# Kernel optimization log

Measured on AMD Instinct MI355X. Metric: run time of the kernel, lower is better.

## Reference

```python
import jax, jax.numpy as jnp
import numpy as np

N = 50000      # num nodes
E = 800000     # num edges (before self-loops)
DIN = 256
DOUT = 256
K = 3


def setup_inputs() -> dict:
    key = jax.random.key(0)
    k1, k2, k3 = jax.random.split(key, 3)
    x = jax.random.normal(k1, (N, DIN), dtype=jnp.float32)
    edge_index = jax.random.randint(k2, (2, E), 0, N, dtype=jnp.int32)
    # xavier_uniform for weight [K+1, DIN, DOUT]
    limit = float(np.sqrt(6.0 / (DIN + DOUT)))
    weight = jax.random.uniform(k3, (K + 1, DIN, DOUT), dtype=jnp.float32,
                                minval=-limit, maxval=limit)
    bias = jnp.zeros((DOUT,), dtype=jnp.float32)
    return {"x": x, "edge_index": edge_index, "weight": weight, "bias": bias}


def reference(x, edge_index, weight, bias):
    num_nodes = x.shape[0]
    # add self loops
    loops = jnp.arange(num_nodes, dtype=edge_index.dtype)
    row = jnp.concatenate([edge_index[0], loops])
    col = jnp.concatenate([edge_index[1], loops])
    # degree of row (including self loops)
    deg = jax.ops.segment_sum(jnp.ones_like(row, dtype=x.dtype), row,
                              num_segments=num_nodes)
    deg_inv_sqrt = jnp.where(deg > 0, jax.lax.rsqrt(jnp.maximum(deg, 1e-30)), 0.0)
    # edge-weighted Laplacian values: -D^{-1/2} A D^{-1/2}, +1 on diagonal
    Lvals = -deg_inv_sqrt[row] * deg_inv_sqrt[col]
    Lvals = jnp.where(row == col, Lvals + 1.0, Lvals)

    def spmm(v):  # [N, D] -> [N, D]
        return jax.ops.segment_sum(Lvals[:, None] * v[col], row,
                                   num_segments=num_nodes)

    out = jnp.matmul(x, weight[0])
    Tx_0 = x
    Tx_1 = spmm(x)
    out = out + jnp.matmul(Tx_1, weight[1])
    for k in range(2, K + 1):
        Tx_2 = 2.0 * spmm(Tx_1) - Tx_0
        out = out + jnp.matmul(Tx_2, weight[k])
        Tx_0, Tx_1 = Tx_1, Tx_2
    return out + bias
```

## Files before the change

### kernel.cpp

```cpp
#include <hip/hip_runtime.h>
#include <hip/hip_bf16.h>

#define DFEAT 256

typedef __attribute__((ext_vector_type(8))) short bf16x8;
typedef __attribute__((ext_vector_type(4))) float f32x4;

__device__ __forceinline__ float bf2f(unsigned short u) {
  return __builtin_bit_cast(float, ((unsigned)u) << 16);
}
__device__ __forceinline__ unsigned short f2bf(float f) {
  __hip_bfloat16 h = __float2bfloat16(f);
  return *reinterpret_cast<unsigned short*>(&h);
}
__device__ __forceinline__ void gload_lds16(const void* g, void* l) {
  __builtin_amdgcn_global_load_lds(
      (const __attribute__((address_space(1))) void*)g,
      (__attribute__((address_space(3))) void*)l, 16, 0, 0);
}


__global__ void k_count(const int* __restrict__ ei0, int E, int* __restrict__ cnt) {
  int i = blockIdx.x * blockDim.x + threadIdx.x;
  if (i < E) atomicAdd(&cnt[ei0[i]], 1);
}

__global__ __launch_bounds__(256) void k_scan1(const int* __restrict__ cnt, int N,
                                               int* __restrict__ incl,
                                               int* __restrict__ bsum,
                                               float* __restrict__ dis) {
  __shared__ int sh[256];
  int t = threadIdx.x;
  int i = blockIdx.x * 256 + t;
  int v = (i < N) ? cnt[i] : 0;
  sh[t] = v;
  __syncthreads();
  for (int o = 1; o < 256; o <<= 1) {
    int u = (t >= o) ? sh[t - o] : 0;
    __syncthreads();
    sh[t] += u;
    __syncthreads();
  }
  if (i < N) {
    incl[i] = sh[t];
    dis[i] = rsqrtf((float)(v + 1));
  }
  if (t == 255) bsum[blockIdx.x] = sh[255];
}

__global__ __launch_bounds__(256) void k_scan2(const int* __restrict__ bsum, int nb,
                                               int* __restrict__ boff) {
  __shared__ int sh[256];
  int t = threadIdx.x;
  int v = (t < nb) ? bsum[t] : 0;
  sh[t] = v;
  __syncthreads();
  for (int o = 1; o < 256; o <<= 1) {
    int u = (t >= o) ? sh[t - o] : 0;
    __syncthreads();
    sh[t] += u;
    __syncthreads();
  }
  if (t < nb) boff[t] = sh[t] - v;
}

__global__ __launch_bounds__(256) void k_scan3(const int* __restrict__ cnt,
                                               const int* __restrict__ incl,
                                               const int* __restrict__ boff, int N, int E,
                                               int* __restrict__ rowptr) {
  int i = blockIdx.x * 256 + threadIdx.x;
  if (i < N) rowptr[i] = boff[blockIdx.x] + incl[i] - cnt[i];
  if (i == 0) rowptr[N] = E;
}

__global__ void k_scatter(const int* __restrict__ ei0, const int* __restrict__ ei1, int E,
                          const int* __restrict__ rowptr, int* __restrict__ cursor,
                          int* __restrict__ cols) {
  int i = blockIdx.x * blockDim.x + threadIdx.x;
  if (i >= E) return;
  int r = ei0[i];
  int pos = rowptr[r] + atomicAdd(&cursor[r], 1);
  cols[pos] = ei1[i];
}


__global__ void k_f2bf(const float* __restrict__ src, unsigned short* __restrict__ dst,
                       int n4) {
  int i = blockIdx.x * blockDim.x + threadIdx.x;
  if (i >= n4) return;
  float4 f = *(const float4*)(src + (size_t)i * 4);
  ushort4 u;
  u.x = f2bf(f.x); u.y = f2bf(f.y); u.z = f2bf(f.z); u.w = f2bf(f.w);
  *(ushort4*)(dst + (size_t)i * 4) = u;
}

__global__ __launch_bounds__(256) void k_wt(const float* __restrict__ W,
                                            unsigned short* __restrict__ WT) {
  int idx = blockIdx.x * 256 + threadIdx.x;
  int n = idx & 255;
  int k = idx >> 8;
  float w0 = W[idx];
  float w1 = W[65536 + idx];
  float w2 = W[2 * 65536 + idx];
  float w3 = W[3 * 65536 + idx];
  int t = (n << 8) | k;
  WT[t]               = f2bf(w0 - w2);
  WT[65536 + t]       = f2bf(w1 - 3.0f * w3);
  WT[2 * 65536 + t]   = f2bf(2.0f * w2);
  WT[3 * 65536 + t]   = f2bf(4.0f * w3);
}


__global__ __launch_bounds__(256) void k_spmm_bf(
    const unsigned short* __restrict__ v, unsigned short* __restrict__ y,
    const int* __restrict__ rowptr, const int* __restrict__ cols,
    const float* __restrict__ dis, int N) {
  int r = blockIdx.x * 4 + (threadIdx.x >> 6);
  if (r >= N) return;
  int lane = threadIdx.x & 63;
  int fo = lane * 4;
  int e0 = rowptr[r], e1 = rowptr[r + 1];
  float dr = dis[r];
  float a0 = 0.f, a1 = 0.f, a2 = 0.f, a3 = 0.f;

  int e = e0;
  for (; e + 1 < e1; e += 2) {
    int cA = cols[e], cB = cols[e + 1];
    float lA = -dr * dis[cA] + (cA == r ? 1.f : 0.f);
    float lB = -dr * dis[cB] + (cB == r ? 1.f : 0.f);
    uint2 uA = *(const uint2*)(v + (size_t)cA * DFEAT + fo);
    uint2 uB = *(const uint2*)(v + (size_t)cB * DFEAT + fo);
    a0 += lA * bf2f(uA.x & 0xffff) + lB * bf2f(uB.x & 0xffff);
    a1 += lA * bf2f(uA.x >> 16)    + lB * bf2f(uB.x >> 16);
    a2 += lA * bf2f(uA.y & 0xffff) + lB * bf2f(uB.y & 0xffff);
    a3 += lA * bf2f(uA.y >> 16)    + lB * bf2f(uB.y >> 16);
  }
  if (e < e1) {
    int c = cols[e];
    float lv = -dr * dis[c] + (c == r ? 1.f : 0.f);
    uint2 u = *(const uint2*)(v + (size_t)c * DFEAT + fo);
    a0 += lv * bf2f(u.x & 0xffff);
    a1 += lv * bf2f(u.x >> 16);
    a2 += lv * bf2f(u.y & 0xffff);
    a3 += lv * bf2f(u.y >> 16);
  }

  float sc = 1.0f - dr * dr;
  uint2 uv = *(const uint2*)(v + (size_t)r * DFEAT + fo);
  a0 += sc * bf2f(uv.x & 0xffff);
  a1 += sc * bf2f(uv.x >> 16);
  a2 += sc * bf2f(uv.y & 0xffff);
  a3 += sc * bf2f(uv.y >> 16);

  uint2 o;
  o.x = (unsigned)f2bf(a0) | ((unsigned)f2bf(a1) << 16);
  o.y = (unsigned)f2bf(a2) | ((unsigned)f2bf(a3) << 16);
  *(uint2*)(y + (size_t)r * DFEAT + fo) = o;
}


__global__ __launch_bounds__(256) void k_gemm4(
    const unsigned short* __restrict__ A0, const unsigned short* __restrict__ A1,
    const unsigned short* __restrict__ A2, const unsigned short* __restrict__ A3,
    const unsigned short* __restrict__ WT,
    const float* __restrict__ bias, float* __restrict__ C, int N) {
  __shared__ __align__(16) unsigned short lds[2][320 * 64];
  int tid = threadIdx.x;
  int lane = tid & 63;
  int w = tid >> 6;
  int brow = blockIdx.x * 64;

  f32x4 acc[4][4] = {};

  int lrow = lane >> 3;
  int sélem = ((lane & 7) ^ lrow) << 3;

  auto stage = [&](int buf, int it) {
    int g = it >> 2;
    int k0 = (it & 3) * 64;
    const unsigned short* Asrc = g == 0 ? A0 : g == 1 ? A1 : g == 2 ? A2 : A3;
    const unsigned short* Bsrc = WT + (g << 16);
#pragma unroll
    for (int c = 0; c < 10; ++c) {
      int gr = c * 32 + w * 8 + lrow;
      const unsigned short* src;
      if (gr < 64) {
        int grow = brow + gr;
        if (grow >= N) grow = N - 1;
        src = Asrc + (size_t)grow * DFEAT + k0 + sélem;
      } else {
        src = Bsrc + (size_t)(gr - 64) * DFEAT + k0 + sélem;
      }
      gload_lds16(src, (char*)lds[buf] + (c * 32 + w * 8) * 128);
    }
  };

  stage(0, 0);
  __syncthreads();

  for (int it = 0; it < 16; ++it) {
    int cur = it & 1;
    if (it < 15) stage(cur ^ 1, it + 1);
#pragma unroll
    for (int ks = 0; ks < 2; ++ks) {
      bf16x8 af[4], bfr[4];
#pragma unroll
      for (int i = 0; i < 4; ++i) {
        int row = i * 16 + (lane & 15);
        int kb = (ks * 64 + ((lane >> 4) << 4)) ^ ((row & 7) << 4);
        af[i] = *(const bf16x8*)((const char*)lds[cur] + row * 128 + kb);
      }
#pragma unroll
      for (int j = 0; j < 4; ++j) {
        int n = w * 64 + j * 16 + (lane & 15);
        int kb = (ks * 64 + ((lane >> 4) << 4)) ^ ((n & 7) << 4);
        bfr[j] = *(const bf16x8*)((const char*)lds[cur] + (64 + n) * 128 + kb);
      }
#pragma unroll
      for (int i = 0; i < 4; ++i)
#pragma unroll
        for (int j = 0; j < 4; ++j)
          acc[i][j] = __builtin_amdgcn_mfma_f32_16x16x32_bf16(af[i], bfr[j], acc[i][j], 0, 0, 0);
    }
    if (it < 15) __syncthreads();
  }

#pragma unroll
  for (int i = 0; i < 4; ++i) {
    int rowb = brow + i * 16 + (lane >> 4) * 4;
#pragma unroll
    for (int j = 0; j < 4; ++j) {
      int col = w * 64 + j * 16 + (lane & 15);
      float b = bias[col];
#pragma unroll
      for (int q = 0; q < 4; ++q) {
        int r = rowb + q;
        if (r < N) C[(size_t)r * DFEAT + col] = acc[i][j][q] + b;
      }
    }
  }
}


extern "C" void kernel_launch(void* const* d_in, const int* in_sizes, int n_in,
                              void* d_out, int out_size, void* d_ws, size_t ws_size,
                              hipStream_t stream) {
  const float* x = (const float*)d_in[0];
  const int* ei = (const int*)d_in[1];
  const float* weight = (const float*)d_in[2];
  const float* bias = (const float*)d_in[3];
  float* out = (float*)d_out;

  int N = in_sizes[0] / DFEAT;
  int E = in_sizes[1] / 2;
  const int* ei0 = ei;
  const int* ei1 = ei + E;

  char* ws = (char*)d_ws;
  size_t off = 0;
  auto alloc = [&](size_t bytes) {
    void* p = ws + off;
    off = (off + bytes + 255) & ~(size_t)255;
    return p;
  };
  int* cnt = (int*)alloc((size_t)2 * N * sizeof(int));
  int* cursor = cnt + N;
  int* rowptr = (int*)alloc((size_t)(N + 1) * sizeof(int));
  float* dis = (float*)alloc((size_t)N * sizeof(float));
  int* cols = (int*)alloc((size_t)E * sizeof(int));
  int* incl = (int*)alloc((size_t)N * sizeof(int));
  int* bsum = (int*)alloc(256 * sizeof(int));
  int* boff = (int*)alloc(256 * sizeof(int));
  unsigned short* xbf = (unsigned short*)alloc((size_t)N * DFEAT * 2);
  unsigned short* S1 = (unsigned short*)alloc((size_t)N * DFEAT * 2);
  unsigned short* S2 = (unsigned short*)alloc((size_t)N * DFEAT * 2);
  unsigned short* S3 = (unsigned short*)alloc((size_t)N * DFEAT * 2);
  unsigned short* WT = (unsigned short*)alloc((size_t)4 * DFEAT * DFEAT * 2);

  hipMemsetAsync(cnt, 0, (size_t)2 * N * sizeof(int), stream);

  int eb = (E + 255) / 256;
  int nb = (N + 255) / 256;
  k_count<<<eb, 256, 0, stream>>>(ei0, E, cnt);
  k_scan1<<<nb, 256, 0, stream>>>(cnt, N, incl, bsum, dis);
  k_scan2<<<1, 256, 0, stream>>>(bsum, nb, boff);
  k_scan3<<<nb, 256, 0, stream>>>(cnt, incl, boff, N, E, rowptr);
  k_scatter<<<eb, 256, 0, stream>>>(ei0, ei1, E, rowptr, cursor, cols);

  int n4 = N * DFEAT / 4;
  k_f2bf<<<(n4 + 255) / 256, 256, 0, stream>>>(x, xbf, n4);
  k_wt<<<DFEAT * DFEAT / 256, 256, 0, stream>>>(weight, WT);

  int sgrid = (N + 3) / 4;
  k_spmm_bf<<<sgrid, 256, 0, stream>>>(xbf, S1, rowptr, cols, dis, N);
  k_spmm_bf<<<sgrid, 256, 0, stream>>>(S1, S2, rowptr, cols, dis, N);
  k_spmm_bf<<<sgrid, 256, 0, stream>>>(S2, S3, rowptr, cols, dis, N);

  int ggrid = (N + 63) / 64;
  k_gemm4<<<ggrid, 256, 0, stream>>>(xbf, S1, S2, S3, WT, bias, out, N);
}
```

Measured before the change: 348.8 us.

## Fuse scan/convert kernels, unroll SpMM edge loop by four, raise MFMA priority

Removes the single-block scan2 kernel by having each scan3 block reduce the preceding block sums itself, and zeroes the scatter cursor there instead of in the memset. Merges the x-to-bf16 conversion and weight transform into one launch. Unrolls the SpMM edge loop from two to four edges so more gathers are in flight, and wraps the MFMA block in s_setprio to favour the matrix work. Together these cut launch count and add memory-level parallelism. The cost is redundant bsum reads in each scan3 block and higher register pressure in SpMM.

Result: faster. 332.3 us (-4.7%).

```diff
diff --git a/kernel.cpp b/kernel.cpp
--- a/kernel.cpp
+++ b/kernel.cpp
@@ -48,28 +48,27 @@
   if (t == 255) bsum[blockIdx.x] = sh[255];
 }
 
-__global__ __launch_bounds__(256) void k_scan2(const int* __restrict__ bsum, int nb,
-                                               int* __restrict__ boff) {
-  __shared__ int sh[256];
-  int t = threadIdx.x;
-  int v = (t < nb) ? bsum[t] : 0;
-  sh[t] = v;
-  __syncthreads();
-  for (int o = 1; o < 256; o <<= 1) {
-    int u = (t >= o) ? sh[t - o] : 0;
-    __syncthreads();
-    sh[t] += u;
-    __syncthreads();
-  }
-  if (t < nb) boff[t] = sh[t] - v;
-}
-
 __global__ __launch_bounds__(256) void k_scan3(const int* __restrict__ cnt,
                                                const int* __restrict__ incl,
-                                               const int* __restrict__ boff, int N, int E,
-                                               int* __restrict__ rowptr) {
-  int i = blockIdx.x * 256 + threadIdx.x;
-  if (i < N) rowptr[i] = boff[blockIdx.x] + incl[i] - cnt[i];
+                                               const int* __restrict__ bsum,
+                                               int N, int E,
+                                               int* __restrict__ rowptr,
+                                               int* __restrict__ cursor) {
+  __shared__ int red[64];
+  int b = blockIdx.x;
+  int t = threadIdx.x;
+  int s = 0;
+  for (int i = t; i < b; i += 256) s += bsum[i];
+#pragma unroll
+  for (int o = 32; o; o >>= 1) s += __shfl_down(s, o);
+  if ((t & 63) == 0) red[t >> 6] = s;
+  __syncthreads();
+  int boff = red[0] + red[1] + red[2] + red[3];
+  int i = b * 256 + t;
+  if (i < N) {
+    rowptr[i] = boff + incl[i] - cnt[i];
+    cursor[i] = 0;
+  }
   if (i == 0) rowptr[N] = E;
 }
 
@@ -84,30 +83,32 @@
 }
 
 
-__global__ void k_f2bf(const float* __restrict__ src, unsigned short* __restrict__ dst,
-                       int n4) {
-  int i = blockIdx.x * blockDim.x + threadIdx.x;
+__global__ __launch_bounds__(256) void k_f2bfwt(const float* __restrict__ x,
+                                                unsigned short* __restrict__ xbf, int n4,
+                                                const float* __restrict__ W,
+                                                unsigned short* __restrict__ WT) {
+  int b = blockIdx.x;
+  if (b < 256) {
+    int idx = b * 256 + threadIdx.x;
+    int n = idx & 255;
+    int k = idx >> 8;
+    float w0 = W[idx];
+    float w1 = W[65536 + idx];
+    float w2 = W[2 * 65536 + idx];
+    float w3 = W[3 * 65536 + idx];
+    int t = (n << 8) | k;
+    WT[t]             = f2bf(w0 - w2);
+    WT[65536 + t]     = f2bf(w1 - 3.0f * w3);
+    WT[2 * 65536 + t] = f2bf(2.0f * w2);
+    WT[3 * 65536 + t] = f2bf(4.0f * w3);
+    return;
+  }
+  int i = (b - 256) * 256 + threadIdx.x;
   if (i >= n4) return;
-  float4 f = *(const float4*)(src + (size_t)i * 4);
+  float4 f = *(const float4*)(x + (size_t)i * 4);
   ushort4 u;
   u.x = f2bf(f.x); u.y = f2bf(f.y); u.z = f2bf(f.z); u.w = f2bf(f.w);
-  *(ushort4*)(dst + (size_t)i * 4) = u;
-}
-
-__global__ __launch_bounds__(256) void k_wt(const float* __restrict__ W,
-                                            unsigned short* __restrict__ WT) {
-  int idx = blockIdx.x * 256 + threadIdx.x;
-  int n = idx & 255;
-  int k = idx >> 8;
-  float w0 = W[idx];
-  float w1 = W[65536 + idx];
-  float w2 = W[2 * 65536 + idx];
-  float w3 = W[3 * 65536 + idx];
-  int t = (n << 8) | k;
-  WT[t]               = f2bf(w0 - w2);
-  WT[65536 + t]       = f2bf(w1 - 3.0f * w3);
-  WT[2 * 65536 + t]   = f2bf(2.0f * w2);
-  WT[3 * 65536 + t]   = f2bf(4.0f * w3);
+  *(ushort4*)(xbf + (size_t)i * 4) = u;
 }
 
 
@@ -124,18 +125,26 @@
   float a0 = 0.f, a1 = 0.f, a2 = 0.f, a3 = 0.f;
 
   int e = e0;
-  for (; e + 1 < e1; e += 2) {
-    int cA = cols[e], cB = cols[e + 1];
-    float lA = -dr * dis[cA] + (cA == r ? 1.f : 0.f);
-    float lB = -dr * dis[cB] + (cB == r ? 1.f : 0.f);
-    uint2 uA = *(const uint2*)(v + (size_t)cA * DFEAT + fo);
-    uint2 uB = *(const uint2*)(v + (size_t)cB * DFEAT + fo);
-    a0 += lA * bf2f(uA.x & 0xffff) + lB * bf2f(uB.x & 0xffff);
-    a1 += lA * bf2f(uA.x >> 16)    + lB * bf2f(uB.x >> 16);
-    a2 += lA * bf2f(uA.y & 0xffff) + lB * bf2f(uB.y & 0xffff);
-    a3 += lA * bf2f(uA.y >> 16)    + lB * bf2f(uB.y >> 16);
-  }
-  if (e < e1) {
+  for (; e + 3 < e1; e += 4) {
+    int c0 = cols[e], c1 = cols[e + 1], c2 = cols[e + 2], c3 = cols[e + 3];
+    float l0 = -dr * dis[c0] + (c0 == r ? 1.f : 0.f);
+    float l1 = -dr * dis[c1] + (c1 == r ? 1.f : 0.f);
+    float l2 = -dr * dis[c2] + (c2 == r ? 1.f : 0.f);
+    float l3 = -dr * dis[c3] + (c3 == r ? 1.f : 0.f);
+    uint2 u0 = *(const uint2*)(v + (size_t)c0 * DFEAT + fo);
+    uint2 u1 = *(const uint2*)(v + (size_t)c1 * DFEAT + fo);
+    uint2 u2 = *(const uint2*)(v + (size_t)c2 * DFEAT + fo);
+    uint2 u3 = *(const uint2*)(v + (size_t)c3 * DFEAT + fo);
+    a0 += l0 * bf2f(u0.x & 0xffff) + l1 * bf2f(u1.x & 0xffff) +
+          l2 * bf2f(u2.x & 0xffff) + l3 * bf2f(u3.x & 0xffff);
+    a1 += l0 * bf2f(u0.x >> 16) + l1 * bf2f(u1.x >> 16) +
+          l2 * bf2f(u2.x >> 16) + l3 * bf2f(u3.x >> 16);
+    a2 += l0 * bf2f(u0.y & 0xffff) + l1 * bf2f(u1.y & 0xffff) +
+          l2 * bf2f(u2.y & 0xffff) + l3 * bf2f(u3.y & 0xffff);
+    a3 += l0 * bf2f(u0.y >> 16) + l1 * bf2f(u1.y >> 16) +
+          l2 * bf2f(u2.y >> 16) + l3 * bf2f(u3.y >> 16);
+  }
+  for (; e < e1; ++e) {
     int c = cols[e];
     float lv = -dr * dis[c] + (c == r ? 1.f : 0.f);
     uint2 u = *(const uint2*)(v + (size_t)c * DFEAT + fo);
@@ -173,7 +182,7 @@
   f32x4 acc[4][4] = {};
 
   int lrow = lane >> 3;
-  int sélem = ((lane & 7) ^ lrow) << 3;
+  int selem = ((lane & 7) ^ lrow) << 3;
 
   auto stage = [&](int buf, int it) {
     int g = it >> 2;
@@ -187,9 +196,9 @@
       if (gr < 64) {
         int grow = brow + gr;
         if (grow >= N) grow = N - 1;
-        src = Asrc + (size_t)grow * DFEAT + k0 + sélem;
+        src = Asrc + (size_t)grow * DFEAT + k0 + selem;
       } else {
-        src = Bsrc + (size_t)(gr - 64) * DFEAT + k0 + sélem;
+        src = Bsrc + (size_t)(gr - 64) * DFEAT + k0 + selem;
       }
       gload_lds16(src, (char*)lds[buf] + (c * 32 + w * 8) * 128);
     }
@@ -216,11 +225,13 @@
         int kb = (ks * 64 + ((lane >> 4) << 4)) ^ ((n & 7) << 4);
         bfr[j] = *(const bf16x8*)((const char*)lds[cur] + (64 + n) * 128 + kb);
       }
+      __builtin_amdgcn_s_setprio(1);
 #pragma unroll
       for (int i = 0; i < 4; ++i)
 #pragma unroll
         for (int j = 0; j < 4; ++j)
           acc[i][j] = __builtin_amdgcn_mfma_f32_16x16x32_bf16(af[i], bfr[j], acc[i][j], 0, 0, 0);
+      __builtin_amdgcn_s_setprio(0);
     }
     if (it < 15) __syncthreads();
   }
@@ -263,33 +274,30 @@
     off = (off + bytes + 255) & ~(size_t)255;
     return p;
   };
-  int* cnt = (int*)alloc((size_t)2 * N * sizeof(int));
-  int* cursor = cnt + N;
+  int* cnt = (int*)alloc((size_t)N * sizeof(int));
+  int* cursor = (int*)alloc((size_t)N * sizeof(int));
   int* rowptr = (int*)alloc((size_t)(N + 1) * sizeof(int));
   float* dis = (float*)alloc((size_t)N * sizeof(float));
   int* cols = (int*)alloc((size_t)E * sizeof(int));
   int* incl = (int*)alloc((size_t)N * sizeof(int));
   int* bsum = (int*)alloc(256 * sizeof(int));
-  int* boff = (int*)alloc(256 * sizeof(int));
   unsigned short* xbf = (unsigned short*)alloc((size_t)N * DFEAT * 2);
   unsigned short* S1 = (unsigned short*)alloc((size_t)N * DFEAT * 2);
   unsigned short* S2 = (unsigned short*)alloc((size_t)N * DFEAT * 2);
   unsigned short* S3 = (unsigned short*)alloc((size_t)N * DFEAT * 2);
   unsigned short* WT = (unsigned short*)alloc((size_t)4 * DFEAT * DFEAT * 2);
 
-  hipMemsetAsync(cnt, 0, (size_t)2 * N * sizeof(int), stream);
+  hipMemsetAsync(cnt, 0, (size_t)N * sizeof(int), stream);
 
   int eb = (E + 255) / 256;
   int nb = (N + 255) / 256;
   k_count<<<eb, 256, 0, stream>>>(ei0, E, cnt);
   k_scan1<<<nb, 256, 0, stream>>>(cnt, N, incl, bsum, dis);
-  k_scan2<<<1, 256, 0, stream>>>(bsum, nb, boff);
-  k_scan3<<<nb, 256, 0, stream>>>(cnt, incl, boff, N, E, rowptr);
+  k_scan3<<<nb, 256, 0, stream>>>(cnt, incl, bsum, N, E, rowptr, cursor);
   k_scatter<<<eb, 256, 0, stream>>>(ei0, ei1, E, rowptr, cursor, cols);
 
   int n4 = N * DFEAT / 4;
-  k_f2bf<<<(n4 + 255) / 256, 256, 0, stream>>>(x, xbf, n4);
-  k_wt<<<DFEAT * DFEAT / 256, 256, 0, stream>>>(weight, WT);
+  k_f2bfwt<<<256 + (n4 + 255) / 256, 256, 0, stream>>>(x, xbf, n4, weight, WT);
 
   int sgrid = (N + 3) / 4;
   k_spmm_bf<<<sgrid, 256, 0, stream>>>(xbf, S1, rowptr, cols, dis, N);
```
